# Performance work log

Measured on AMD Instinct MI355X. Metric: run time of the kernel, lower is better.

The kernel has to match this reference:

```python
import jax, jax.numpy as jnp
import numpy as np

EMBED_DIM = 1024
N_HEADS = 16
HEAD_DIM = EMBED_DIM // N_HEADS
N_CATS = 5
SCALE = float(np.sqrt(HEAD_DIM))


def setup_inputs() -> dict:
    key = jax.random.key(0)
    ks = jax.random.split(key, 16)
    B, S = 2, 2048
    inp = {
        "query": jax.random.normal(ks[0], (B, S, EMBED_DIM), jnp.float32),
        "key_": jax.random.normal(ks[1], (B, S, EMBED_DIM), jnp.float32),
        "value": jax.random.normal(ks[2], (B, S, EMBED_DIM), jnp.float32),
        "responses": jax.random.randint(ks[3], (B, S), 0, N_CATS),
        "mask": jnp.ones((B, S, S), jnp.int32),
        # Linear params (torch convention: y = x @ W.T + b)
        "Wq": jax.random.normal(ks[4], (EMBED_DIM, EMBED_DIM), jnp.float32) * 0.02,
        "bq": jnp.zeros((EMBED_DIM,), jnp.float32),
        "Wk": jax.random.normal(ks[5], (EMBED_DIM, EMBED_DIM), jnp.float32) * 0.02,
        "bk": jnp.zeros((EMBED_DIM,), jnp.float32),
        "Wv": jax.random.normal(ks[6], (EMBED_DIM, EMBED_DIM), jnp.float32) * 0.02,
        "bv": jnp.zeros((EMBED_DIM,), jnp.float32),
        "Wo": jax.random.normal(ks[7], (EMBED_DIM, EMBED_DIM), jnp.float32) * 0.02,
        "bo": jnp.zeros((EMBED_DIM,), jnp.float32),
        # qwk_modulation: Linear(1, n_heads)
        "Wm": jax.random.normal(ks[8], (N_HEADS, 1), jnp.float32) * 0.5,
        "bm": jnp.zeros((N_HEADS,), jnp.float32),
    }
    return inp


def _qwk_matrix():
    i = jnp.arange(N_CATS, dtype=jnp.float32)
    return 1.0 - (i[:, None] - i[None, :]) ** 2 / (N_CATS - 1) ** 2  # [C, C]


def reference(query, key_, value, responses, mask,
              Wq, bq, Wk, bk, Wv, bv, Wo, bo, Wm, bm):
    B, S, E = query.shape
    # projections
    Q = (query @ Wq.T + bq).reshape(B, S, N_HEADS, HEAD_DIM).transpose(0, 2, 1, 3)
    K = (key_ @ Wk.T + bk).reshape(B, S, N_HEADS, HEAD_DIM).transpose(0, 2, 1, 3)
    V = (value @ Wv.T + bv).reshape(B, S, N_HEADS, HEAD_DIM).transpose(0, 2, 1, 3)
    scores = jnp.einsum("bhqd,bhkd->bhqk", Q, K) / SCALE  # [B,H,S,S]
    # QWK ordinal bias: gather pairwise weight, tiny linear 1->H, broadcast-add
    qwk = _qwk_matrix()
    pair = qwk[responses[:, :, None], responses[:, None, :]]  # [B,S,S]
    # Linear(1, n_heads): bias[...,None] @ Wm.T + bm -> [B,S,S,H] -> [B,H,S,S]
    head_bias = pair[:, None, :, :] * Wm[:, 0][None, :, None, None] + bm[None, :, None, None]
    scores = scores + head_bias
    scores = jnp.where(mask[:, None, :, :] == 0, -1e9, scores)
    attn = jax.nn.softmax(scores, axis=-1)
    attended = jnp.einsum("bhqk,bhkd->bhqd", attn, V)
    attended = attended.transpose(0, 2, 1, 3).reshape(B, S, E)
    return attended @ Wo.T + bo
```

## Files before the change

### kernel.cpp

```cpp
#include <hip/hip_runtime.h>
#include <hip/hip_bf16.h>
#include <stdint.h>

#define S_LEN 2048
#define EMB   1024
#define NHEAD 16
#define HDIM  64
#define BATCH 2

typedef __bf16 bf16x8 __attribute__((ext_vector_type(8)));
typedef float  f32x4  __attribute__((ext_vector_type(4)));

__device__ __forceinline__ void gll16(const void* g, void* l) {
  __builtin_amdgcn_global_load_lds(
      (const __attribute__((address_space(1))) void*)g,
      (__attribute__((address_space(3))) void*)l,
      16, 0, 0);
}

__global__ void __launch_bounds__(256) cast_mask_kernel(
    const float* __restrict__ s0, const float* __restrict__ s1, const float* __restrict__ s2,
    const float* __restrict__ s3, const float* __restrict__ s4, const float* __restrict__ s5,
    const float* __restrict__ s6,
    __hip_bfloat16* __restrict__ d0, __hip_bfloat16* __restrict__ d1,
    __hip_bfloat16* __restrict__ d2, __hip_bfloat16* __restrict__ d3,
    __hip_bfloat16* __restrict__ d4, __hip_bfloat16* __restrict__ d5,
    __hip_bfloat16* __restrict__ d6,
    const int* __restrict__ mask, unsigned* __restrict__ flags) {
  const int z = blockIdx.y;
  const int t = threadIdx.x;
  if (z == 7) {
    const int kt = blockIdx.x & 15, qt = (blockIdx.x >> 4) & 31, b = (int)blockIdx.x >> 9;
    const int* base = mask + ((size_t)b * S_LEN + (size_t)qt * 64) * S_LEN + (size_t)kt * 128;
    int ok = 1;
#pragma unroll
    for (int p = 0; p < 8; ++p) {
      int idx = p * 256 + t;
      int row = idx >> 5, c4 = idx & 31;
      const int4 v = *(const int4*)(base + (size_t)row * S_LEN + c4 * 4);
      ok &= (v.x != 0) & (v.y != 0) & (v.z != 0) & (v.w != 0);
    }
    unsigned long long bl = __ballot(ok);
    __shared__ unsigned long long bw[4];
    bw[t >> 6] = bl;
    __syncthreads();
    if (t == 0) {
      unsigned all = ((bw[0] & bw[1] & bw[2] & bw[3]) == ~0ull) ? 1u : 0u;
      flags[((size_t)b * 32 + qt) * 16 + kt] = all;
    }
    return;
  }
  const float* s = (z == 0) ? s0 : (z == 1) ? s1 : (z == 2) ? s2 : (z == 3) ? s3
                 : (z == 4) ? s4 : (z == 5) ? s5 : s6;
  __hip_bfloat16* d = (z == 0) ? d0 : (z == 1) ? d1 : (z == 2) ? d2 : (z == 3) ? d3
                    : (z == 4) ? d4 : (z == 5) ? d5 : d6;
  const int n = (z < 3) ? (BATCH * S_LEN * EMB) : (EMB * EMB);
  const size_t i = ((size_t)blockIdx.x * 256 + t) * 16;
  if (i >= (size_t)n) return;
  __hip_bfloat16 tmp[16];
#pragma unroll
  for (int j = 0; j < 4; ++j) {
    const float4 v = *(const float4*)(s + i + j * 4);
    tmp[j * 4 + 0] = __float2bfloat16(v.x);
    tmp[j * 4 + 1] = __float2bfloat16(v.y);
    tmp[j * 4 + 2] = __float2bfloat16(v.z);
    tmp[j * 4 + 3] = __float2bfloat16(v.w);
  }
  *(bf16x8*)(d + i)     = *(bf16x8*)&tmp[0];
  *(bf16x8*)(d + i + 8) = *(bf16x8*)&tmp[8];
}

__global__ void __launch_bounds__(256, 2)
gemm_kernel(const __hip_bfloat16* __restrict__ A0, const __hip_bfloat16* __restrict__ A1,
            const __hip_bfloat16* __restrict__ A2,
            const __hip_bfloat16* __restrict__ W0, const __hip_bfloat16* __restrict__ W1,
            const __hip_bfloat16* __restrict__ W2,
            const float* __restrict__ b0, const float* __restrict__ b1,
            const float* __restrict__ b2,
            __hip_bfloat16* __restrict__ O0, __hip_bfloat16* __restrict__ O1,
            __hip_bfloat16* __restrict__ O2) {
  __shared__ __align__(16) __hip_bfloat16 As[128 * 64];
  __shared__ __align__(16) __hip_bfloat16 Bs[128 * 64];

  const int L = blockIdx.x;
  const int m0 = (L & 31) * 128;
  const int n0 = ((L >> 5) & 7) * 128;
  const int z  = L >> 8;

  const __hip_bfloat16* A  = (z == 0) ? A0 : ((z == 1) ? A1 : A2);
  const __hip_bfloat16* W  = (z == 0) ? W0 : ((z == 1) ? W1 : W2);
  const float* bi          = (z == 0) ? b0 : ((z == 1) ? b1 : b2);
  __hip_bfloat16* O        = (z == 0) ? O0 : ((z == 1) ? O1 : O2);

  const int t = threadIdx.x;
  const int w = t >> 6, lane = t & 63, quad = lane >> 4, l15 = lane & 15;
  const int wr = w >> 1, wc = w & 1;

  f32x4 acc[4][4];
#pragma unroll
  for (int i = 0; i < 4; ++i)
#pragma unroll
    for (int j = 0; j < 4; ++j) acc[i][j] = (f32x4)0.0f;

  const int srow = t >> 3;
  const int scb  = (t & 7) ^ (srow & 7);
  const __hip_bfloat16* Ap = A + (size_t)(m0 + srow) * EMB + (scb << 3);
  const __hip_bfloat16* Wp = W + (size_t)(n0 + srow) * EMB + (scb << 3);

  for (int k0 = 0; k0 < EMB; k0 += 64) {
    __syncthreads();
#pragma unroll
    for (int rnd = 0; rnd < 4; ++rnd) {
      gll16(Ap + (size_t)(rnd * 32) * EMB + k0, &As[(rnd * 256 + (w << 6)) * 8]);
      gll16(Wp + (size_t)(rnd * 32) * EMB + k0, &Bs[(rnd * 256 + (w << 6)) * 8]);
    }
    __syncthreads();

    bf16x8 af[4][2], bfr[4][2];
#pragma unroll
    for (int i = 0; i < 4; ++i) {
      const int ra = wr * 64 + i * 16 + l15;
#pragma unroll
      for (int hh = 0; hh < 2; ++hh)
        af[i][hh] = *(const bf16x8*)&As[ra * 64 + ((((hh << 2) + quad) ^ (l15 & 7)) << 3)];
    }
#pragma unroll
    for (int j = 0; j < 4; ++j) {
      const int rbw = wc * 64 + j * 16 + l15;
#pragma unroll
      for (int hh = 0; hh < 2; ++hh)
        bfr[j][hh] = *(const bf16x8*)&Bs[rbw * 64 + ((((hh << 2) + quad) ^ (l15 & 7)) << 3)];
    }
#pragma unroll
    for (int hh = 0; hh < 2; ++hh)
#pragma unroll
      for (int i = 0; i < 4; ++i)
#pragma unroll
        for (int j = 0; j < 4; ++j)
          acc[i][j] =
              __builtin_amdgcn_mfma_f32_16x16x32_bf16(af[i][hh], bfr[j][hh], acc[i][j], 0, 0, 0);
  }

#pragma unroll
  for (int j = 0; j < 4; ++j) {
    const int ng = n0 + wc * 64 + j * 16 + l15;
    const float bb = bi[ng];
    const int h = ng >> 6, d = ng & 63;
#pragma unroll
    for (int i = 0; i < 4; ++i) {
#pragma unroll
      for (int r = 0; r < 4; ++r) {
        const int mg = m0 + wr * 64 + i * 16 + quad * 4 + r;
        const int b = mg >> 11, s = mg & 2047;
        float v = acc[i][j][r] + bb;
        if (z == 0) {
          O[(((size_t)b * NHEAD + h) * S_LEN + s) * HDIM + d] =
              __float2bfloat16(v * (0.125f * 1.4426950408889634f));
        } else if (z == 1) {
          O[(((size_t)b * NHEAD + h) * S_LEN + s) * HDIM + d] = __float2bfloat16(v);
        } else {
          const size_t idx = (size_t)(b * NHEAD + h) * 131072 + (size_t)(s >> 7) * 8192 +
                             (size_t)((((s >> 5) & 3) * 4 + ((s >> 2) & 3)) * 64 + d) * 8 +
                             ((s >> 4) & 1) * 4 + (s & 3);
          O[idx] = __float2bfloat16(v);
        }
      }
    }
  }
}

__global__ void __launch_bounds__(256, 2)
gemm_o_kernel(const __hip_bfloat16* __restrict__ A, const __hip_bfloat16* __restrict__ W,
              const float* __restrict__ bi, float* __restrict__ O) {
  __shared__ __align__(16) __hip_bfloat16 As[64 * 64];
  __shared__ __align__(16) __hip_bfloat16 Bs[128 * 64];
  const int L = blockIdx.x;
  const int m0 = (L & 63) * 64;
  const int n0 = (L >> 6) * 128;
  const int t = threadIdx.x;
  const int w = t >> 6, lane = t & 63, quad = lane >> 4, l15 = lane & 15;
  const int wr = w >> 1, wc = w & 1;

  f32x4 acc[2][4];
#pragma unroll
  for (int i = 0; i < 2; ++i)
#pragma unroll
    for (int j = 0; j < 4; ++j) acc[i][j] = (f32x4)0.0f;

  const int srow = t >> 3;
  const int scb  = (t & 7) ^ (srow & 7);
  const __hip_bfloat16* Ap = A + (size_t)(m0 + srow) * EMB + (scb << 3);
  const __hip_bfloat16* Wp = W + (size_t)(n0 + srow) * EMB + (scb << 3);

  for (int k0 = 0; k0 < EMB; k0 += 64) {
    __syncthreads();
#pragma unroll
    for (int rnd = 0; rnd < 2; ++rnd)
      gll16(Ap + (size_t)(rnd * 32) * EMB + k0, &As[(rnd * 256 + (w << 6)) * 8]);
#pragma unroll
    for (int rnd = 0; rnd < 4; ++rnd)
      gll16(Wp + (size_t)(rnd * 32) * EMB + k0, &Bs[(rnd * 256 + (w << 6)) * 8]);
    __syncthreads();

    bf16x8 af[2][2], bfr[4][2];
#pragma unroll
    for (int i = 0; i < 2; ++i) {
      const int ra = wr * 32 + i * 16 + l15;
#pragma unroll
      for (int hh = 0; hh < 2; ++hh)
        af[i][hh] = *(const bf16x8*)&As[ra * 64 + ((((hh << 2) + quad) ^ (l15 & 7)) << 3)];
    }
#pragma unroll
    for (int j = 0; j < 4; ++j) {
      const int rbw = wc * 64 + j * 16 + l15;
#pragma unroll
      for (int hh = 0; hh < 2; ++hh)
        bfr[j][hh] = *(const bf16x8*)&Bs[rbw * 64 + ((((hh << 2) + quad) ^ (l15 & 7)) << 3)];
    }
#pragma unroll
    for (int hh = 0; hh < 2; ++hh)
#pragma unroll
      for (int i = 0; i < 2; ++i)
#pragma unroll
        for (int j = 0; j < 4; ++j)
          acc[i][j] =
              __builtin_amdgcn_mfma_f32_16x16x32_bf16(af[i][hh], bfr[j][hh], acc[i][j], 0, 0, 0);
  }

#pragma unroll
  for (int j = 0; j < 4; ++j) {
    const int ng = n0 + wc * 64 + j * 16 + l15;
    const float bb = bi[ng];
#pragma unroll
    for (int i = 0; i < 2; ++i) {
#pragma unroll
      for (int r = 0; r < 4; ++r) {
        const int mg = m0 + wr * 32 + i * 16 + quad * 4 + r;
        O[(size_t)mg * EMB + ng] = acc[i][j][r] + bb;
      }
    }
  }
}

__global__ void __launch_bounds__(512, 4)
flash_kernel(const __hip_bfloat16* __restrict__ qws, const __hip_bfloat16* __restrict__ kws,
             const __hip_bfloat16* __restrict__ vpk, const int* __restrict__ responses,
             const int* __restrict__ mask, const float* __restrict__ Wm,
             const unsigned* __restrict__ flags, __hip_bfloat16* __restrict__ att) {
  __shared__ __align__(16) unsigned char smem[32768];
  __shared__ unsigned char rb[S_LEN];
  __shared__ float lsm[512];

  __hip_bfloat16* Ks = (__hip_bfloat16*)smem;
  __hip_bfloat16* Vs = (__hip_bfloat16*)(smem + 16384);
  float* sm = (float*)smem;

  const int t = threadIdx.x;
  const int w = t >> 6, lane = t & 63, quad = lane >> 4, l15 = lane & 15;
  const int L = blockIdx.x;
  const int bh = L & 31;
  const int qt = L >> 5;
  const int b = bh >> 4, h = bh & 15;
  const int q0 = qt * 128;
  const int wq = w & 3, khalf = w >> 2;

#pragma unroll
  for (int i = 0; i < 4; ++i)
    rb[i * 512 + t] = (unsigned char)responses[b * S_LEN + i * 512 + t];

  const __hip_bfloat16* qbase = qws + ((size_t)bh * S_LEN + q0 + wq * 32) * HDIM;
  bf16x8 qf[2][2];
#pragma unroll
  for (int qg = 0; qg < 2; ++qg)
#pragma unroll
    for (int ks = 0; ks < 2; ++ks)
      qf[qg][ks] =
          *(const bf16x8*)(qbase + (size_t)(qg * 16 + l15) * HDIM + ks * 32 + quad * 8);

  const float c = Wm[h] * (0.0625f * 1.4426950408889634f);
  float A2[2];
#pragma unroll
  for (int qg = 0; qg < 2; ++qg)
    A2[qg] = 2.0f * c * (float)responses[b * S_LEN + q0 + wq * 32 + qg * 16 + l15];

  const __hip_bfloat16* kptr = kws + ((size_t)bh * S_LEN + (t >> 3)) * HDIM +
                               (((t & 7) ^ ((t >> 3) & 7)) << 3);
  const __hip_bfloat16* vptr = vpk + (size_t)bh * 131072 + (size_t)t * 8;

  float lsum[2] = {0.f, 0.f};
  f32x4 acc_o[2][4];
#pragma unroll
  for (int qg = 0; qg < 2; ++qg)
#pragma unroll
    for (int dt = 0; dt < 4; ++dt) acc_o[qg][dt] = (f32x4)0.0f;

  for (int kt = 0; kt < S_LEN / 128; ++kt) {
    __syncthreads();
#pragma unroll
    for (int p = 0; p < 2; ++p) {
      gll16(kptr + p * 64 * HDIM, &Ks[(p * 512 + (w << 6)) * 8]);
      gll16(vptr + p * 4096,      &Vs[(p * 512 + (w << 6)) * 8]);
    }
    kptr += 128 * HDIM;
    vptr += 8192;
    __syncthreads();

    const unsigned fl = flags[((size_t)b * 32 + 2 * qt + (wq >> 1)) * 16 + kt];

    bf16x8 pfr[2][2];
#pragma unroll
    for (int ct = 0; ct < 4; ++ct) {
      const int rowk = khalf * 64 + ct * 16 + l15;
      bf16x8 kf0 = *(const bf16x8*)&Ks[rowk * 64 + ((quad ^ (l15 & 7)) << 3)];
      bf16x8 kf1 = *(const bf16x8*)&Ks[rowk * 64 + (((4 + quad) ^ (l15 & 7)) << 3)];
      const unsigned ru = *(const unsigned*)&rb[kt * 128 + khalf * 64 + ct * 16 + quad * 4];
#pragma unroll
      for (int qg = 0; qg < 2; ++qg) {
        f32x4 sc = __builtin_amdgcn_mfma_f32_16x16x32_bf16(kf0, qf[qg][0], (f32x4)0.0f, 0, 0, 0);
        sc = __builtin_amdgcn_mfma_f32_16x16x32_bf16(kf1, qf[qg][1], sc, 0, 0, 0);
        __hip_bfloat16 pb[4];
#pragma unroll
        for (int r = 0; r < 4; ++r) {
          const float rkf = (float)((ru >> (8 * r)) & 255u);
          const float sb = fmaf(rkf, fmaf(-c, rkf, A2[qg]), sc[r]);
          float p = __builtin_amdgcn_exp2f(sb);
          if (!fl) {
            int mq = mask[((size_t)b * S_LEN + q0 + wq * 32 + qg * 16 + l15) * S_LEN +
                          kt * 128 + khalf * 64 + ct * 16 + quad * 4 + r];
            p = mq ? p : 0.0f;
          }
          lsum[qg] += p;
          pb[r] = __float2bfloat16(p);
        }
        __hip_bfloat16* half = (__hip_bfloat16*)&pfr[qg][ct >> 1] + (ct & 1) * 4;
        half[0] = pb[0]; half[1] = pb[1]; half[2] = pb[2]; half[3] = pb[3];
      }
    }

#pragma unroll
    for (int ct2 = 0; ct2 < 2; ++ct2) {
      const int g2 = khalf * 2 + ct2;
#pragma unroll
      for (int dt = 0; dt < 4; ++dt) {
        bf16x8 vv = *(const bf16x8*)&Vs[(((g2 << 2) + quad) * 64 + (dt << 4) + l15) << 3];
#pragma unroll
        for (int qg = 0; qg < 2; ++qg)
          acc_o[qg][dt] =
              __builtin_amdgcn_mfma_f32_16x16x32_bf16(pfr[qg][ct2], vv, acc_o[qg][dt], 0, 0, 0);
      }
    }
  }

  __syncthreads();
  if (khalf == 0) {
#pragma unroll
    for (int qg = 0; qg < 2; ++qg) {
#pragma unroll
      for (int dt = 0; dt < 4; ++dt)
        *(f32x4*)&sm[((((wq << 1) + qg) << 2) + dt) * 256 + lane * 4] = acc_o[qg][dt];
      lsm[((wq << 1) + qg) * 64 + lane] = lsum[qg];
    }
  }
  __syncthreads();
  if (khalf == 1) {
#pragma unroll
    for (int qg = 0; qg < 2; ++qg) {
      lsum[qg] += lsm[((wq << 1) + qg) * 64 + lane];
      lsum[qg] += __shfl_xor(lsum[qg], 16, 64);
      lsum[qg] += __shfl_xor(lsum[qg], 32, 64);
#pragma unroll
      for (int dt = 0; dt < 4; ++dt)
        acc_o[qg][dt] += *(const f32x4*)&sm[((((wq << 1) + qg) << 2) + dt) * 256 + lane * 4];
      float inv[4];
#pragma unroll
      for (int r = 0; r < 4; ++r) inv[r] = 1.0f / __shfl(lsum[qg], quad * 4 + r, 64);
#pragma unroll
      for (int dt = 0; dt < 4; ++dt)
#pragma unroll
        for (int r = 0; r < 4; ++r)
          att[((size_t)b * S_LEN + q0 + wq * 32 + qg * 16 + quad * 4 + r) * EMB +
              h * HDIM + dt * 16 + l15] = __float2bfloat16(acc_o[qg][dt][r] * inv[r]);
    }
  }
}

extern "C" void kernel_launch(void* const* d_in, const int* in_sizes, int n_in,
                              void* d_out, int out_size, void* d_ws, size_t ws_size,
                              hipStream_t stream) {
  const float* query = (const float*)d_in[0];
  const float* key_  = (const float*)d_in[1];
  const float* value = (const float*)d_in[2];
  const int* responses = (const int*)d_in[3];
  const int* mask      = (const int*)d_in[4];
  const float* Wq = (const float*)d_in[5];
  const float* bq = (const float*)d_in[6];
  const float* Wk = (const float*)d_in[7];
  const float* bk = (const float*)d_in[8];
  const float* Wv = (const float*)d_in[9];
  const float* bv = (const float*)d_in[10];
  const float* Wo = (const float*)d_in[11];
  const float* bo = (const float*)d_in[12];
  const float* Wm = (const float*)d_in[13];

  __hip_bfloat16* ws = (__hip_bfloat16*)d_ws;
  const size_t NTOK = (size_t)BATCH * S_LEN * EMB;
  const size_t NW   = (size_t)EMB * EMB;
  __hip_bfloat16* qcast = ws;
  __hip_bfloat16* kcast = ws + NTOK;
  __hip_bfloat16* vcast = ws + 2 * NTOK;
  __hip_bfloat16* wqb   = ws + 3 * NTOK;
  __hip_bfloat16* wkb   = wqb + NW;
  __hip_bfloat16* wvb   = wqb + 2 * NW;
  __hip_bfloat16* wob   = wqb + 3 * NW;
  __hip_bfloat16* qws   = wqb + 4 * NW;
  __hip_bfloat16* kws   = qws + NTOK;
  __hip_bfloat16* vpk   = qws + 2 * NTOK;
  __hip_bfloat16* att   = qws + 3 * NTOK;
  unsigned* flags       = (unsigned*)(qws + 4 * NTOK);
  float* out            = (float*)d_out;

  cast_mask_kernel<<<dim3(1024, 8), 256, 0, stream>>>(
      query, key_, value, Wq, Wk, Wv, Wo,
      qcast, kcast, vcast, wqb, wkb, wvb, wob, mask, flags);
  gemm_kernel<<<768, 256, 0, stream>>>(qcast, kcast, vcast, wqb, wkb, wvb,
                                       bq, bk, bv, qws, kws, vpk);
  flash_kernel<<<512, 512, 0, stream>>>(qws, kws, vpk, responses, mask,
                                        Wm, flags, att);
  gemm_o_kernel<<<512, 256, 0, stream>>>(att, wob, bo, out);
}
```

Measured before the change: 249.6 us.

## Fuse fp32-to-bf16 casts into GEMMs and shrink flash attention blocks

Removes the separate cast kernel. The QKV and output GEMMs now load fp32 inputs and weights straight into LDS and convert them to bf16 in registers before the MFMAs, and the mask-flag scan moves into the QKV kernel's grid. This drops a full read/write pass over activations and weights, plus one launch, at the cost of twice the LDS traffic per k-step and extra conversion ALU work. The flash kernel moves to 256-thread blocks with 64 query rows each, doubling the grid, and computes row sums with an MFMA against a ones vector instead of scalar adds and shuffles.

```diff
diff --git a/kernel.cpp b/kernel.cpp
--- a/kernel.cpp
+++ b/kernel.cpp
@@ -18,19 +18,32 @@
       16, 0, 0);
 }
 
-__global__ void __launch_bounds__(256) cast_mask_kernel(
-    const float* __restrict__ s0, const float* __restrict__ s1, const float* __restrict__ s2,
-    const float* __restrict__ s3, const float* __restrict__ s4, const float* __restrict__ s5,
-    const float* __restrict__ s6,
-    __hip_bfloat16* __restrict__ d0, __hip_bfloat16* __restrict__ d1,
-    __hip_bfloat16* __restrict__ d2, __hip_bfloat16* __restrict__ d3,
-    __hip_bfloat16* __restrict__ d4, __hip_bfloat16* __restrict__ d5,
-    __hip_bfloat16* __restrict__ d6,
-    const int* __restrict__ mask, unsigned* __restrict__ flags) {
-  const int z = blockIdx.y;
+__device__ __forceinline__ bf16x8 pack_bf16(f32x4 a, f32x4 b) {
+  __hip_bfloat16 tmp[8];
+#pragma unroll
+  for (int k = 0; k < 4; ++k) { tmp[k] = __float2bfloat16(a[k]); tmp[4 + k] = __float2bfloat16(b[k]); }
+  return *(bf16x8*)tmp;
+}
+
+__global__ void __launch_bounds__(256, 3)
+qkv_flags_kernel(const float* __restrict__ A0, const float* __restrict__ A1,
+                 const float* __restrict__ A2,
+                 const float* __restrict__ W0, const float* __restrict__ W1,
+                 const float* __restrict__ W2,
+                 const float* __restrict__ b0, const float* __restrict__ b1,
+                 const float* __restrict__ b2,
+                 __hip_bfloat16* __restrict__ O0, __hip_bfloat16* __restrict__ O1,
+                 __hip_bfloat16* __restrict__ O2,
+                 const int* __restrict__ mask, unsigned* __restrict__ flags) {
+  __shared__ __align__(16) float Asf[128 * 32];
+  __shared__ __align__(16) float Bsf[128 * 32];
+  __shared__ unsigned long long bw[4];
+
+  const int L = blockIdx.x;
   const int t = threadIdx.x;
-  if (z == 7) {
-    const int kt = blockIdx.x & 15, qt = (blockIdx.x >> 4) & 31, b = (int)blockIdx.x >> 9;
+
+  if (L < 1024) {
+    const int kt = L & 15, qt = (L >> 4) & 31, b = L >> 9;
     const int* base = mask + ((size_t)b * S_LEN + (size_t)qt * 64) * S_LEN + (size_t)kt * 128;
     int ok = 1;
 #pragma unroll
@@ -41,7 +54,6 @@
       ok &= (v.x != 0) & (v.y != 0) & (v.z != 0) & (v.w != 0);
     }
     unsigned long long bl = __ballot(ok);
-    __shared__ unsigned long long bw[4];
     bw[t >> 6] = bl;
     __syncthreads();
     if (t == 0) {
@@ -50,49 +62,17 @@
     }
     return;
   }
-  const float* s = (z == 0) ? s0 : (z == 1) ? s1 : (z == 2) ? s2 : (z == 3) ? s3
-                 : (z == 4) ? s4 : (z == 5) ? s5 : s6;
-  __hip_bfloat16* d = (z == 0) ? d0 : (z == 1) ? d1 : (z == 2) ? d2 : (z == 3) ? d3
-                    : (z == 4) ? d4 : (z == 5) ? d5 : d6;
-  const int n = (z < 3) ? (BATCH * S_LEN * EMB) : (EMB * EMB);
-  const size_t i = ((size_t)blockIdx.x * 256 + t) * 16;
-  if (i >= (size_t)n) return;
-  __hip_bfloat16 tmp[16];
-#pragma unroll
-  for (int j = 0; j < 4; ++j) {
-    const float4 v = *(const float4*)(s + i + j * 4);
-    tmp[j * 4 + 0] = __float2bfloat16(v.x);
-    tmp[j * 4 + 1] = __float2bfloat16(v.y);
-    tmp[j * 4 + 2] = __float2bfloat16(v.z);
-    tmp[j * 4 + 3] = __float2bfloat16(v.w);
-  }
-  *(bf16x8*)(d + i)     = *(bf16x8*)&tmp[0];
-  *(bf16x8*)(d + i + 8) = *(bf16x8*)&tmp[8];
-}
-
-__global__ void __launch_bounds__(256, 2)
-gemm_kernel(const __hip_bfloat16* __restrict__ A0, const __hip_bfloat16* __restrict__ A1,
-            const __hip_bfloat16* __restrict__ A2,
-            const __hip_bfloat16* __restrict__ W0, const __hip_bfloat16* __restrict__ W1,
-            const __hip_bfloat16* __restrict__ W2,
-            const float* __restrict__ b0, const float* __restrict__ b1,
-            const float* __restrict__ b2,
-            __hip_bfloat16* __restrict__ O0, __hip_bfloat16* __restrict__ O1,
-            __hip_bfloat16* __restrict__ O2) {
-  __shared__ __align__(16) __hip_bfloat16 As[128 * 64];
-  __shared__ __align__(16) __hip_bfloat16 Bs[128 * 64];
-
-  const int L = blockIdx.x;
-  const int m0 = (L & 31) * 128;
-  const int n0 = ((L >> 5) & 7) * 128;
-  const int z  = L >> 8;
-
-  const __hip_bfloat16* A  = (z == 0) ? A0 : ((z == 1) ? A1 : A2);
-  const __hip_bfloat16* W  = (z == 0) ? W0 : ((z == 1) ? W1 : W2);
-  const float* bi          = (z == 0) ? b0 : ((z == 1) ? b1 : b2);
-  __hip_bfloat16* O        = (z == 0) ? O0 : ((z == 1) ? O1 : O2);
-
-  const int t = threadIdx.x;
+
+  const int G = L - 1024;
+  const int m0 = (G & 31) * 128;
+  const int n0 = ((G >> 5) & 7) * 128;
+  const int z  = G >> 8;
+
+  const float* A  = (z == 0) ? A0 : ((z == 1) ? A1 : A2);
+  const float* W  = (z == 0) ? W0 : ((z == 1) ? W1 : W2);
+  const float* bi = (z == 0) ? b0 : ((z == 1) ? b1 : b2);
+  __hip_bfloat16* O = (z == 0) ? O0 : ((z == 1) ? O1 : O2);
+
   const int w = t >> 6, lane = t & 63, quad = lane >> 4, l15 = lane & 15;
   const int wr = w >> 1, wc = w & 1;
 
@@ -104,41 +84,38 @@
 
   const int srow = t >> 3;
   const int scb  = (t & 7) ^ (srow & 7);
-  const __hip_bfloat16* Ap = A + (size_t)(m0 + srow) * EMB + (scb << 3);
-  const __hip_bfloat16* Wp = W + (size_t)(n0 + srow) * EMB + (scb << 3);
-
-  for (int k0 = 0; k0 < EMB; k0 += 64) {
+  const float* Ap = A + (size_t)(m0 + srow) * EMB + scb * 4;
+  const float* Wp = W + (size_t)(n0 + srow) * EMB + scb * 4;
+
+  for (int k0 = 0; k0 < EMB; k0 += 32) {
     __syncthreads();
 #pragma unroll
     for (int rnd = 0; rnd < 4; ++rnd) {
-      gll16(Ap + (size_t)(rnd * 32) * EMB + k0, &As[(rnd * 256 + (w << 6)) * 8]);
-      gll16(Wp + (size_t)(rnd * 32) * EMB + k0, &Bs[(rnd * 256 + (w << 6)) * 8]);
-    }
-    __syncthreads();
-
-    bf16x8 af[4][2], bfr[4][2];
+      gll16(Ap + (size_t)(rnd * 32) * EMB + k0, &Asf[(rnd * 256 + (w << 6)) * 4]);
+      gll16(Wp + (size_t)(rnd * 32) * EMB + k0, &Bsf[(rnd * 256 + (w << 6)) * 4]);
+    }
+    __syncthreads();
+
+    bf16x8 af[4], bfr[4];
 #pragma unroll
     for (int i = 0; i < 4; ++i) {
       const int ra = wr * 64 + i * 16 + l15;
-#pragma unroll
-      for (int hh = 0; hh < 2; ++hh)
-        af[i][hh] = *(const bf16x8*)&As[ra * 64 + ((((hh << 2) + quad) ^ (l15 & 7)) << 3)];
+      f32x4 a0 = *(const f32x4*)&Asf[ra * 32 + ((((quad << 1)) ^ (ra & 7)) << 2)];
+      f32x4 a1 = *(const f32x4*)&Asf[ra * 32 + ((((quad << 1) | 1) ^ (ra & 7)) << 2)];
+      af[i] = pack_bf16(a0, a1);
     }
 #pragma unroll
     for (int j = 0; j < 4; ++j) {
-      const int rbw = wc * 64 + j * 16 + l15;
-#pragma unroll
-      for (int hh = 0; hh < 2; ++hh)
-        bfr[j][hh] = *(const bf16x8*)&Bs[rbw * 64 + ((((hh << 2) + quad) ^ (l15 & 7)) << 3)];
-    }
-#pragma unroll
-    for (int hh = 0; hh < 2; ++hh)
-#pragma unroll
-      for (int i = 0; i < 4; ++i)
-#pragma unroll
-        for (int j = 0; j < 4; ++j)
-          acc[i][j] =
-              __builtin_amdgcn_mfma_f32_16x16x32_bf16(af[i][hh], bfr[j][hh], acc[i][j], 0, 0, 0);
+      const int rb_ = wc * 64 + j * 16 + l15;
+      f32x4 b0v = *(const f32x4*)&Bsf[rb_ * 32 + ((((quad << 1)) ^ (rb_ & 7)) << 2)];
+      f32x4 b1v = *(const f32x4*)&Bsf[rb_ * 32 + ((((quad << 1) | 1) ^ (rb_ & 7)) << 2)];
+      bfr[j] = pack_bf16(b0v, b1v);
+    }
+#pragma unroll
+    for (int i = 0; i < 4; ++i)
+#pragma unroll
+      for (int j = 0; j < 4; ++j)
+        acc[i][j] = __builtin_amdgcn_mfma_f32_16x16x32_bf16(af[i], bfr[j], acc[i][j], 0, 0, 0);
   }
 
 #pragma unroll
@@ -170,10 +147,10 @@
 }
 
 __global__ void __launch_bounds__(256, 2)
-gemm_o_kernel(const __hip_bfloat16* __restrict__ A, const __hip_bfloat16* __restrict__ W,
+gemm_o_kernel(const __hip_bfloat16* __restrict__ A, const float* __restrict__ W,
               const float* __restrict__ bi, float* __restrict__ O) {
-  __shared__ __align__(16) __hip_bfloat16 As[64 * 64];
-  __shared__ __align__(16) __hip_bfloat16 Bs[128 * 64];
+  __shared__ __align__(16) __hip_bfloat16 Asb[64 * 32];
+  __shared__ __align__(16) float Bsf[128 * 32];
   const int L = blockIdx.x;
   const int m0 = (L & 63) * 64;
   const int n0 = (L >> 6) * 128;
@@ -187,44 +164,35 @@
 #pragma unroll
     for (int j = 0; j < 4; ++j) acc[i][j] = (f32x4)0.0f;
 
-  const int srow = t >> 3;
-  const int scb  = (t & 7) ^ (srow & 7);
-  const __hip_bfloat16* Ap = A + (size_t)(m0 + srow) * EMB + (scb << 3);
-  const __hip_bfloat16* Wp = W + (size_t)(n0 + srow) * EMB + (scb << 3);
-
-  for (int k0 = 0; k0 < EMB; k0 += 64) {
-    __syncthreads();
-#pragma unroll
-    for (int rnd = 0; rnd < 2; ++rnd)
-      gll16(Ap + (size_t)(rnd * 32) * EMB + k0, &As[(rnd * 256 + (w << 6)) * 8]);
+  const int srW = t >> 3;
+  const int scbW = (t & 7) ^ (srW & 7);
+  const __hip_bfloat16* Ap = A + (size_t)(m0 + (t >> 2)) * EMB + (t & 3) * 8;
+  const float* Wp = W + (size_t)(n0 + srW) * EMB + scbW * 4;
+
+  for (int k0 = 0; k0 < EMB; k0 += 32) {
+    __syncthreads();
+    gll16(Ap + k0, &Asb[(w << 6) * 8]);
 #pragma unroll
     for (int rnd = 0; rnd < 4; ++rnd)
-      gll16(Wp + (size_t)(rnd * 32) * EMB + k0, &Bs[(rnd * 256 + (w << 6)) * 8]);
-    __syncthreads();
-
-    bf16x8 af[2][2], bfr[4][2];
-#pragma unroll
-    for (int i = 0; i < 2; ++i) {
-      const int ra = wr * 32 + i * 16 + l15;
-#pragma unroll
-      for (int hh = 0; hh < 2; ++hh)
-        af[i][hh] = *(const bf16x8*)&As[ra * 64 + ((((hh << 2) + quad) ^ (l15 & 7)) << 3)];
-    }
+      gll16(Wp + (size_t)(rnd * 32) * EMB + k0, &Bsf[(rnd * 256 + (w << 6)) * 4]);
+    __syncthreads();
+
+    bf16x8 af[2], bfr[4];
+#pragma unroll
+    for (int i = 0; i < 2; ++i)
+      af[i] = *(const bf16x8*)&Asb[(wr * 32 + i * 16 + l15) * 32 + quad * 8];
 #pragma unroll
     for (int j = 0; j < 4; ++j) {
-      const int rbw = wc * 64 + j * 16 + l15;
-#pragma unroll
-      for (int hh = 0; hh < 2; ++hh)
-        bfr[j][hh] = *(const bf16x8*)&Bs[rbw * 64 + ((((hh << 2) + quad) ^ (l15 & 7)) << 3)];
-    }
-#pragma unroll
-    for (int hh = 0; hh < 2; ++hh)
-#pragma unroll
-      for (int i = 0; i < 2; ++i)
-#pragma unroll
-        for (int j = 0; j < 4; ++j)
-          acc[i][j] =
-              __builtin_amdgcn_mfma_f32_16x16x32_bf16(af[i][hh], bfr[j][hh], acc[i][j], 0, 0, 0);
+      const int rb_ = wc * 64 + j * 16 + l15;
+      f32x4 b0v = *(const f32x4*)&Bsf[rb_ * 32 + ((((quad << 1)) ^ (rb_ & 7)) << 2)];
+      f32x4 b1v = *(const f32x4*)&Bsf[rb_ * 32 + ((((quad << 1) | 1) ^ (rb_ & 7)) << 2)];
+      bfr[j] = pack_bf16(b0v, b1v);
+    }
+#pragma unroll
+    for (int i = 0; i < 2; ++i)
+#pragma unroll
+      for (int j = 0; j < 4; ++j)
+        acc[i][j] = __builtin_amdgcn_mfma_f32_16x16x32_bf16(af[i], bfr[j], acc[i][j], 0, 0, 0);
   }
 
 #pragma unroll
@@ -242,18 +210,18 @@
   }
 }
 
-__global__ void __launch_bounds__(512, 4)
+__global__ void __launch_bounds__(256, 4)
 flash_kernel(const __hip_bfloat16* __restrict__ qws, const __hip_bfloat16* __restrict__ kws,
              const __hip_bfloat16* __restrict__ vpk, const int* __restrict__ responses,
              const int* __restrict__ mask, const float* __restrict__ Wm,
              const unsigned* __restrict__ flags, __hip_bfloat16* __restrict__ att) {
   __shared__ __align__(16) unsigned char smem[32768];
   __shared__ unsigned char rb[S_LEN];
-  __shared__ float lsm[512];
 
   __hip_bfloat16* Ks = (__hip_bfloat16*)smem;
   __hip_bfloat16* Vs = (__hip_bfloat16*)(smem + 16384);
-  float* sm = (float*)smem;
+  float* sm  = (float*)smem;
+  float* lsm = sm + 4096;
 
   const int t = threadIdx.x;
   const int w = t >> 6, lane = t & 63, quad = lane >> 4, l15 = lane & 15;
@@ -261,12 +229,12 @@
   const int bh = L & 31;
   const int qt = L >> 5;
   const int b = bh >> 4, h = bh & 15;
-  const int q0 = qt * 128;
-  const int wq = w & 3, khalf = w >> 2;
-
-#pragma unroll
-  for (int i = 0; i < 4; ++i)
-    rb[i * 512 + t] = (unsigned char)responses[b * S_LEN + i * 512 + t];
+  const int q0 = qt * 64;
+  const int wq = w & 1, khalf = w >> 1;
+
+#pragma unroll
+  for (int i = 0; i < 8; ++i)
+    rb[i * 256 + t] = (unsigned char)responses[b * S_LEN + i * 256 + t];
 
   const __hip_bfloat16* qbase = qws + ((size_t)bh * S_LEN + q0 + wq * 32) * HDIM;
   bf16x8 qf[2][2];
@@ -287,25 +255,34 @@
                                (((t & 7) ^ ((t >> 3) & 7)) << 3);
   const __hip_bfloat16* vptr = vpk + (size_t)bh * 131072 + (size_t)t * 8;
 
-  float lsum[2] = {0.f, 0.f};
+  bf16x8 onesf;
+  {
+    __hip_bfloat16 one = __float2bfloat16(1.0f);
+#pragma unroll
+    for (int k = 0; k < 8; ++k) ((__hip_bfloat16*)&onesf)[k] = one;
+  }
+
+  f32x4 acc_l[2];
   f32x4 acc_o[2][4];
 #pragma unroll
-  for (int qg = 0; qg < 2; ++qg)
+  for (int qg = 0; qg < 2; ++qg) {
+    acc_l[qg] = (f32x4)0.0f;
 #pragma unroll
     for (int dt = 0; dt < 4; ++dt) acc_o[qg][dt] = (f32x4)0.0f;
+  }
 
   for (int kt = 0; kt < S_LEN / 128; ++kt) {
     __syncthreads();
 #pragma unroll
-    for (int p = 0; p < 2; ++p) {
-      gll16(kptr + p * 64 * HDIM, &Ks[(p * 512 + (w << 6)) * 8]);
-      gll16(vptr + p * 4096,      &Vs[(p * 512 + (w << 6)) * 8]);
+    for (int p = 0; p < 4; ++p) {
+      gll16(kptr + p * 32 * HDIM, &Ks[(p * 256 + (w << 6)) * 8]);
+      gll16(vptr + p * 2048,      &Vs[(p * 256 + (w << 6)) * 8]);
     }
     kptr += 128 * HDIM;
     vptr += 8192;
     __syncthreads();
 
-    const unsigned fl = flags[((size_t)b * 32 + 2 * qt + (wq >> 1)) * 16 + kt];
+    const unsigned fl = flags[((size_t)b * 32 + qt) * 16 + kt];
 
     bf16x8 pfr[2][2];
 #pragma unroll
@@ -329,7 +306,6 @@
                           kt * 128 + khalf * 64 + ct * 16 + quad * 4 + r];
             p = mq ? p : 0.0f;
           }
-          lsum[qg] += p;
           pb[r] = __float2bfloat16(p);
         }
         __hip_bfloat16* half = (__hip_bfloat16*)&pfr[qg][ct >> 1] + (ct & 1) * 4;
@@ -341,6 +317,9 @@
     for (int ct2 = 0; ct2 < 2; ++ct2) {
       const int g2 = khalf * 2 + ct2;
 #pragma unroll
+      for (int qg = 0; qg < 2; ++qg)
+        acc_l[qg] = __builtin_amdgcn_mfma_f32_16x16x32_bf16(pfr[qg][ct2], onesf, acc_l[qg], 0, 0, 0);
+#pragma unroll
       for (int dt = 0; dt < 4; ++dt) {
         bf16x8 vv = *(const bf16x8*)&Vs[(((g2 << 2) + quad) * 64 + (dt << 4) + l15) << 3];
 #pragma unroll
@@ -358,28 +337,25 @@
 #pragma unroll
       for (int dt = 0; dt < 4; ++dt)
         *(f32x4*)&sm[((((wq << 1) + qg) << 2) + dt) * 256 + lane * 4] = acc_o[qg][dt];
-      lsm[((wq << 1) + qg) * 64 + lane] = lsum[qg];
+      if (l15 == 0) *(f32x4*)&lsm[((wq << 1) + qg) * 16 + quad * 4] = acc_l[qg];
     }
   }
   __syncthreads();
   if (khalf == 1) {
 #pragma unroll
     for (int qg = 0; qg < 2; ++qg) {
-      lsum[qg] += lsm[((wq << 1) + qg) * 64 + lane];
-      lsum[qg] += __shfl_xor(lsum[qg], 16, 64);
-      lsum[qg] += __shfl_xor(lsum[qg], 32, 64);
-#pragma unroll
-      for (int dt = 0; dt < 4; ++dt)
+      acc_l[qg] += *(const f32x4*)&lsm[((wq << 1) + qg) * 16 + quad * 4];
+      float inv[4];
+#pragma unroll
+      for (int r = 0; r < 4; ++r) inv[r] = 1.0f / acc_l[qg][r];
+#pragma unroll
+      for (int dt = 0; dt < 4; ++dt) {
         acc_o[qg][dt] += *(const f32x4*)&sm[((((wq << 1) + qg) << 2) + dt) * 256 + lane * 4];
-      float inv[4];
-#pragma unroll
-      for (int r = 0; r < 4; ++r) inv[r] = 1.0f / __shfl(lsum[qg], quad * 4 + r, 64);
-#pragma unroll
-      for (int dt = 0; dt < 4; ++dt)
 #pragma unroll
         for (int r = 0; r < 4; ++r)
           att[((size_t)b * S_LEN + q0 + wq * 32 + qg * 16 + quad * 4 + r) * EMB +
               h * HDIM + dt * 16 + l15] = __float2bfloat16(acc_o[qg][dt][r] * inv[r]);
+      }
     }
   }
 }
@@ -404,27 +380,16 @@
 
   __hip_bfloat16* ws = (__hip_bfloat16*)d_ws;
   const size_t NTOK = (size_t)BATCH * S_LEN * EMB;
-  const size_t NW   = (size_t)EMB * EMB;
-  __hip_bfloat16* qcast = ws;
-  __hip_bfloat16* kcast = ws + NTOK;
-  __hip_bfloat16* vcast = ws + 2 * NTOK;
-  __hip_bfloat16* wqb   = ws + 3 * NTOK;
-  __hip_bfloat16* wkb   = wqb + NW;
-  __hip_bfloat16* wvb   = wqb + 2 * NW;
-  __hip_bfloat16* wob   = wqb + 3 * NW;
-  __hip_bfloat16* qws   = wqb + 4 * NW;
-  __hip_bfloat16* kws   = qws + NTOK;
-  __hip_bfloat16* vpk   = qws + 2 * NTOK;
-  __hip_bfloat16* att   = qws + 3 * NTOK;
-  unsigned* flags       = (unsigned*)(qws + 4 * NTOK);
-  float* out            = (float*)d_out;
-
-  cast_mask_kernel<<<dim3(1024, 8), 256, 0, stream>>>(
-      query, key_, value, Wq, Wk, Wv, Wo,
-      qcast, kcast, vcast, wqb, wkb, wvb, wob, mask, flags);
-  gemm_kernel<<<768, 256, 0, stream>>>(qcast, kcast, vcast, wqb, wkb, wvb,
-                                       bq, bk, bv, qws, kws, vpk);
-  flash_kernel<<<512, 512, 0, stream>>>(qws, kws, vpk, responses, mask,
-                                        Wm, flags, att);
-  gemm_o_kernel<<<512, 256, 0, stream>>>(att, wob, bo, out);
-}
+  __hip_bfloat16* qws  = ws;
+  __hip_bfloat16* kws  = ws + NTOK;
+  __hip_bfloat16* vpk  = ws + 2 * NTOK;
+  __hip_bfloat16* att  = ws + 3 * NTOK;
+  unsigned* flags      = (unsigned*)(ws + 4 * NTOK);
+  float* out           = (float*)d_out;
+
+  qkv_flags_kernel<<<1792, 256, 0, stream>>>(query, key_, value, Wq, Wk, Wv,
+                                             bq, bk, bv, qws, kws, vpk, mask, flags);
+  flash_kernel<<<1024, 256, 0, stream>>>(qws, kws, vpk, responses, mask,
+                                         Wm, flags, att);
+  gemm_o_kernel<<<512, 256, 0, stream>>>(att, Wo, bo, out);
+}
```

After: 281.5 us. +12.8%, slower.
